# Kernel optimization log

Measured on AMD Instinct MI355X. Metric: run time of the kernel, lower is better.

Reference implementation:

```python
import jax, jax.numpy as jnp
import numpy as np

H = 1024; NH = 16; HD = H // NH  # hidden, heads, head_dim

def setup_inputs() -> dict:
    key = jax.random.key(0)
    ks = jax.random.split(key, 9)
    s = 1.0 / np.sqrt(H)
    return {
        "hidden_states": jax.random.normal(ks[0], (2, 2048, H), jnp.float32),
        "Wq": jax.random.uniform(ks[1], (H, H), jnp.float32, -s, s),
        "bq": jnp.zeros((H,), jnp.float32),
        "Wk": jax.random.uniform(ks[2], (H, H), jnp.float32, -s, s),
        "bk": jnp.zeros((H,), jnp.float32),
        "Wv": jax.random.uniform(ks[3], (H, H), jnp.float32, -s, s),
        "bv": jnp.zeros((H,), jnp.float32),
        "Wo": jax.random.uniform(ks[4], (H, H), jnp.float32, -s, s),
        "bo": jnp.zeros((H,), jnp.float32),
    }

def reference(hidden_states, Wq, bq, Wk, bk, Wv, bv, Wo, bo):
    B, S, _ = hidden_states.shape
    def heads(x):  # [B,S,H] -> [B,NH,S,HD]
        return x.reshape(B, S, NH, HD).transpose(0, 2, 1, 3)
    q = heads(hidden_states @ Wq + bq)
    k = heads(hidden_states @ Wk + bk)
    v = heads(hidden_states @ Wv + bv)
    scores = jnp.einsum('bhqd,bhkd->bhqk', q, k) / jnp.sqrt(jnp.float32(HD))
    causal = jnp.where(jnp.tril(jnp.ones((S, S), bool)), 0.0, -jnp.inf)
    probs = jax.nn.softmax(scores + causal[None, None], axis=-1)
    ctx = jnp.einsum('bhqk,bhkd->bhqd', probs, v)
    ctx = ctx.transpose(0, 2, 1, 3).reshape(B, S, H)
    return ctx @ Wo + bo
```

## Files before the change

### kernel.cpp

```cpp
#include <hip/hip_runtime.h>
#include <hip/hip_bf16.h>

#define BB 2
#define SS 2048
#define HH 1024
#define NHH 16
#define HDD 64
#define MM (BB*SS)
#define QKV_N (3*HH)

typedef _Float16 f16x8 __attribute__((ext_vector_type(8)));
typedef _Float16 f16x4 __attribute__((ext_vector_type(4)));
typedef float f32x4 __attribute__((ext_vector_type(4)));

#define MFMA16(a,b,c)  __builtin_amdgcn_mfma_f32_16x16x32_f16((a),(b),(c),0,0,0)
#define MFMA16K16(a,b,c) __builtin_amdgcn_mfma_f32_16x16x16f16((a),(b),(c),0,0,0)

__device__ __forceinline__ void gl2lds16(const _Float16* g, _Float16* l) {
    __builtin_amdgcn_global_load_lds(
        (const __attribute__((address_space(1))) void*)g,
        (__attribute__((address_space(3))) void*)l, 16, 0, 0);
}

__device__ __forceinline__ float fexp2(float x) { return __builtin_amdgcn_exp2f(x); }

__global__ __launch_bounds__(256) void prep_kernel(
    const float* __restrict__ X,
    const float* __restrict__ W0, const float* __restrict__ W1,
    const float* __restrict__ W2, const float* __restrict__ W3,
    _Float16* __restrict__ Xh,
    _Float16* __restrict__ WqkvT, _Float16* __restrict__ WoT)
{
    __shared__ float t[64][65];
    int z = blockIdx.z;
    int tid = threadIdx.x;
    if (z == 4) {
        int base = (blockIdx.y * 16 + blockIdx.x) * 256 + tid;
        const float4* xin = (const float4*)X;
        f16x4* xout = (f16x4*)Xh;
#pragma unroll
        for (int i = 0; i < 16; ++i) {
            float4 v = xin[base + i * 65536];
            f16x4 hh = {(_Float16)v.x, (_Float16)v.y, (_Float16)v.z, (_Float16)v.w};
            xout[base + i * 65536] = hh;
        }
        return;
    }
    const float* src = (z == 0) ? W0 : (z == 1) ? W1 : (z == 2) ? W2 : W3;
    _Float16* dst = (z < 3) ? (WqkvT + (size_t)z * HH * HH) : WoT;
    int k0 = blockIdx.y * 64, n0 = blockIdx.x * 64;
#pragma unroll
    for (int p = 0; p < 4; ++p) {
        int row = p * 16 + (tid >> 4);
        int col4 = (tid & 15) * 4;
        float4 v = *(const float4*)&src[(size_t)(k0 + row) * HH + n0 + col4];
        t[row][col4 + 0] = v.x; t[row][col4 + 1] = v.y;
        t[row][col4 + 2] = v.z; t[row][col4 + 3] = v.w;
    }
    __syncthreads();
#pragma unroll
    for (int p = 0; p < 2; ++p) {
        int nc = p * 32 + (tid >> 3);
        int ch = tid & 7;
        f16x8 o;
#pragma unroll
        for (int j = 0; j < 8; ++j) o[j] = (_Float16)t[ch * 8 + j][nc];
        *(f16x8*)&dst[(size_t)(n0 + nc) * HH + k0 + ch * 8] = o;
    }
}

__global__ __launch_bounds__(512, 2) void gemm_qkv_kernel(
    const _Float16* __restrict__ A, const _Float16* __restrict__ Bt,
    const float* __restrict__ bias0, const float* __restrict__ bias1, const float* __restrict__ bias2,
    _Float16* __restrict__ Qh, _Float16* __restrict__ Kh, _Float16* __restrict__ Vt)
{
    __shared__ _Float16 smem[65536];

    int bid = blockIdx.y * 12 + blockIdx.x;
    int swzb = (bid & 7) * 24 + (bid >> 3);
    int bx = swzb % 12, by = swzb / 12;
    int row0 = by * 256, n0 = bx * 256;

    int tid = threadIdx.x;
    int w = tid >> 6, l = tid & 63, m16 = l & 15, quad = l >> 4;
    int wm = w >> 2, wn = w & 3;

    int srow = w * 16 + (l >> 2);
    int sch = (l & 3) ^ ((l >> 2) & 3) ^ ((l >> 4) & 3);
    const _Float16* aptr = A + (size_t)(row0 + srow) * HH + sch * 8;
    const _Float16* bptr = Bt + (size_t)(n0 + srow) * HH + sch * 8;

    int gsw = (m16 & 3) ^ ((m16 >> 2) & 3);
    int acol = (quad ^ gsw) * 8;

    f32x4 zero4 = {0.f, 0.f, 0.f, 0.f};
    f32x4 acc[8][4];
#pragma unroll
    for (int i = 0; i < 8; ++i)
#pragma unroll
        for (int j = 0; j < 4; ++j) acc[i][j] = zero4;

    auto stageA = [&](int s, int h, int ks) {
        gl2lds16(aptr + (size_t)h * 128 * HH + s * 64 + ks * 32,
                 smem + (s & 1) * 16384 + ks * 8192 + (h * 128 + w * 16) * 32);
    };
    auto stageB = [&](int s, int h, int ks) {
        gl2lds16(bptr + (size_t)h * 128 * HH + s * 64 + ks * 32,
                 smem + 32768 + (s & 1) * 16384 + ks * 8192 + (h * 128 + w * 16) * 32);
    };

    stageA(0, 0, 0); stageA(0, 0, 1); stageA(0, 1, 0); stageA(0, 1, 1);
    stageB(0, 0, 0); stageB(0, 0, 1); stageB(0, 1, 0); stageB(0, 1, 1);

    for (int s = 0; s < 16; ++s) {
        const _Float16* Ab = smem + (s & 1) * 16384;
        const _Float16* Bb = smem + 32768 + (s & 1) * 16384;
        bool pf = (s + 1 < 16);
        f16x8 af[4][2], bf[2][2];

        if (pf) { stageA(s + 1, 0, 0); stageA(s + 1, 0, 1);
                  asm volatile("s_waitcnt vmcnt(2)" ::: "memory"); }
        else    { asm volatile("s_waitcnt vmcnt(0)" ::: "memory"); }
        asm volatile("s_barrier" ::: "memory");
#pragma unroll
        for (int fi = 0; fi < 4; ++fi)
#pragma unroll
            for (int ks = 0; ks < 2; ++ks)
                af[fi][ks] = *(const f16x8*)&Ab[ks * 8192 + (wm * 128 + fi * 16 + m16) * 32 + acol];
#pragma unroll
        for (int fj = 0; fj < 2; ++fj)
#pragma unroll
            for (int ks = 0; ks < 2; ++ks)
                bf[fj][ks] = *(const f16x8*)&Bb[ks * 8192 + (wn * 64 + fj * 16 + m16) * 32 + acol];
        __builtin_amdgcn_s_setprio(1);
#pragma unroll
        for (int fi = 0; fi < 4; ++fi)
#pragma unroll
            for (int fj = 0; fj < 2; ++fj) {
                acc[fi][fj] = MFMA16(af[fi][0], bf[fj][0], acc[fi][fj]);
                acc[fi][fj] = MFMA16(af[fi][1], bf[fj][1], acc[fi][fj]);
            }
        __builtin_amdgcn_s_setprio(0);
        asm volatile("s_barrier" ::: "memory");

        if (pf) { stageA(s + 1, 1, 0); stageA(s + 1, 1, 1); }
#pragma unroll
        for (int fj = 0; fj < 2; ++fj)
#pragma unroll
            for (int ks = 0; ks < 2; ++ks)
                bf[fj][ks] = *(const f16x8*)&Bb[ks * 8192 + (wn * 64 + 32 + fj * 16 + m16) * 32 + acol];
        __builtin_amdgcn_s_setprio(1);
#pragma unroll
        for (int fi = 0; fi < 4; ++fi)
#pragma unroll
            for (int fj = 0; fj < 2; ++fj) {
                acc[fi][2 + fj] = MFMA16(af[fi][0], bf[fj][0], acc[fi][2 + fj]);
                acc[fi][2 + fj] = MFMA16(af[fi][1], bf[fj][1], acc[fi][2 + fj]);
            }
        __builtin_amdgcn_s_setprio(0);
        asm volatile("s_barrier" ::: "memory");

        if (pf) { stageB(s + 1, 0, 0); stageB(s + 1, 0, 1); }
#pragma unroll
        for (int fi = 0; fi < 4; ++fi)
#pragma unroll
            for (int ks = 0; ks < 2; ++ks)
                af[fi][ks] = *(const f16x8*)&Ab[ks * 8192 + (wm * 128 + 64 + fi * 16 + m16) * 32 + acol];
        __builtin_amdgcn_s_setprio(1);
#pragma unroll
        for (int fi = 0; fi < 4; ++fi)
#pragma unroll
            for (int fj = 0; fj < 2; ++fj) {
                acc[4 + fi][2 + fj] = MFMA16(af[fi][0], bf[fj][0], acc[4 + fi][2 + fj]);
                acc[4 + fi][2 + fj] = MFMA16(af[fi][1], bf[fj][1], acc[4 + fi][2 + fj]);
            }
        __builtin_amdgcn_s_setprio(0);
        asm volatile("s_barrier" ::: "memory");

        if (pf) { stageB(s + 1, 1, 0); stageB(s + 1, 1, 1); }
#pragma unroll
        for (int fj = 0; fj < 2; ++fj)
#pragma unroll
            for (int ks = 0; ks < 2; ++ks)
                bf[fj][ks] = *(const f16x8*)&Bb[ks * 8192 + (wn * 64 + fj * 16 + m16) * 32 + acol];
        __builtin_amdgcn_s_setprio(1);
#pragma unroll
        for (int fi = 0; fi < 4; ++fi)
#pragma unroll
            for (int fj = 0; fj < 2; ++fj) {
                acc[4 + fi][fj] = MFMA16(af[fi][0], bf[fj][0], acc[4 + fi][fj]);
                acc[4 + fi][fj] = MFMA16(af[fi][1], bf[fj][1], acc[4 + fi][fj]);
            }
        __builtin_amdgcn_s_setprio(0);
        asm volatile("s_barrier" ::: "memory");
    }

    int which = n0 >> 10;
    const float* bias = (which == 0) ? bias0 : (which == 1) ? bias1 : bias2;
    int b = row0 >> 11, s0 = row0 & 2047;

#pragma unroll
    for (int rh = 0; rh < 2; ++rh) {
        __syncthreads();
        if (wm == rh) {
#pragma unroll
            for (int j = 0; j < 4; ++j) {
                int n_local = wn * 64 + j * 16 + m16;
                float bi = bias[(n0 + n_local) & 1023];
#pragma unroll
                for (int i = 0; i < 8; ++i)
#pragma unroll
                    for (int r = 0; r < 4; ++r) {
                        int m_loc = i * 16 + quad * 4 + r;
                        float v = acc[i][j][r] + bi;
                        if (which == 0) v *= 0.18033688011112042f;
                        if (which == 2) smem[n_local * 136 + m_loc] = (_Float16)v;
                        else            smem[m_loc * 264 + n_local] = (_Float16)v;
                    }
            }
        }
        __syncthreads();
        int hs0 = s0 + rh * 128;
        if (which == 2) {
#pragma unroll
            for (int p = 0; p < 8; ++p) {
                int n_local = p * 32 + (tid >> 4);
                int schunk = tid & 15;
                f16x8 v = *(const f16x8*)&smem[n_local * 136 + schunk * 8];
                int nw = (n0 + n_local) & 1023;
                int hh = nw >> 6, d = nw & 63;
                *(f16x8*)&Vt[((size_t)(b * NHH + hh) * HDD + d) * SS + hs0 + schunk * 8] = v;
            }
        } else {
            _Float16* dst = (which == 0) ? Qh : Kh;
            int hh0 = (n0 & 1023) >> 6;
#pragma unroll
            for (int p = 0; p < 8; ++p) {
                int m_local = p * 16 + (tid >> 5);
                int seg = tid & 31;
                f16x8 v = *(const f16x8*)&smem[m_local * 264 + seg * 8];
                int hh = hh0 + (seg >> 3), d = (seg & 7) * 8;
                *(f16x8*)&dst[((size_t)(b * NHH + hh) * SS + hs0 + m_local) * HDD + d] = v;
            }
        }
    }
}

__global__ __launch_bounds__(256) void gemm_out_kernel(
    const _Float16* __restrict__ A, const _Float16* __restrict__ Bt,
    const float* __restrict__ bias0, float* __restrict__ Out)
{
    const int K = HH;
    const int NT = K / 32;
    __shared__ _Float16 smem[24576];

    int row0 = blockIdx.y * 128, n0 = blockIdx.x * 128;
    int tid = threadIdx.x;
    int w = tid >> 6, l = tid & 63, m16 = l & 15, quad = l >> 4;
    int wm = w >> 1, wn = w & 1;

    int srow = w * 32 + (l >> 2);
    int sch = (l & 3) ^ ((l >> 2) & 3) ^ ((l >> 4) & 3);
    const _Float16* aptr = A + (size_t)(row0 + srow) * K + sch * 8;
    const _Float16* bptr = Bt + (size_t)(n0 + srow) * K + sch * 8;

    int gsw = (m16 & 3) ^ ((m16 >> 2) & 3);
    int acol = (quad ^ gsw) * 8;

    f32x4 zero4 = {0.f, 0.f, 0.f, 0.f};
    f32x4 acc[4][4];
#pragma unroll
    for (int i = 0; i < 4; ++i)
#pragma unroll
        for (int j = 0; j < 4; ++j) acc[i][j] = zero4;

    auto stage = [&](int t, int s) {
        int k0 = t * 32;
        int ao = s * 4096 + (w * 32) * 32;
        int bo = 12288 + s * 4096 + (w * 32) * 32;
        gl2lds16(aptr + k0, smem + ao);
        gl2lds16(aptr + (size_t)16 * K + k0, smem + ao + 16 * 32);
        gl2lds16(bptr + k0, smem + bo);
        gl2lds16(bptr + (size_t)16 * K + k0, smem + bo + 16 * 32);
    };

    stage(0, 0);
    stage(1, 1);
    int cur = 0;
    for (int t = 0; t < NT; ++t) {
        if (t < NT - 1) asm volatile("s_waitcnt vmcnt(4)" ::: "memory");
        else            asm volatile("s_waitcnt vmcnt(0)" ::: "memory");
        asm volatile("s_barrier" ::: "memory");
        if (t + 2 < NT) {
            int nxt = cur + 2; if (nxt >= 3) nxt -= 3;
            stage(t + 2, nxt);
        }
        const _Float16* Asr = smem + cur * 4096;
        const _Float16* Bsr = smem + 12288 + cur * 4096;
        f16x8 af[4], bf[4];
#pragma unroll
        for (int i = 0; i < 4; ++i)
            af[i] = *(const f16x8*)&Asr[(wm * 64 + i * 16 + m16) * 32 + acol];
#pragma unroll
        for (int j = 0; j < 4; ++j)
            bf[j] = *(const f16x8*)&Bsr[(wn * 64 + j * 16 + m16) * 32 + acol];
#pragma unroll
        for (int i = 0; i < 4; ++i)
#pragma unroll
            for (int j = 0; j < 4; ++j)
                acc[i][j] = MFMA16(af[i], bf[j], acc[i][j]);
        cur = (cur == 2) ? 0 : cur + 1;
    }

#pragma unroll
    for (int j = 0; j < 4; ++j) {
        int n = n0 + wn * 64 + j * 16 + m16;
        float bi = bias0[n];
#pragma unroll
        for (int i = 0; i < 4; ++i)
#pragma unroll
            for (int r = 0; r < 4; ++r) {
                int mg = row0 + wm * 64 + i * 16 + quad * 4 + r;
                Out[(size_t)mg * HH + n] = acc[i][j][r] + bi;
            }
    }
}

__global__ __launch_bounds__(512, 4) void attn_kernel(
    const _Float16* __restrict__ Qh, const _Float16* __restrict__ Kh,
    const _Float16* __restrict__ Vt, _Float16* __restrict__ Ctx)
{
    __shared__ _Float16 KV[3 * 8192];

    int tid = threadIdx.x;
    int w = tid >> 6, l = tid & 63;
    int m16 = l & 15, quad = l >> 4;
    int b = blockIdx.z, h = blockIdx.y;
    int tA = blockIdx.x, tB = 31 - tA;
    int half = w >> 2, wq = w & 3;
    int myT = half ? tB : tA;

    const _Float16* Q = Qh + (size_t)(b * NHH + h) * SS * HDD;
    const _Float16* K = Kh + (size_t)(b * NHH + h) * SS * HDD;
    const _Float16* V = Vt + (size_t)(b * NHH + h) * HDD * SS;

    int q = myT * 64 + wq * 16 + m16;
    f16x8 aq0 = *(const f16x8*)(Q + (size_t)q * HDD + quad * 8);
    f16x8 aq1 = *(const f16x8*)(Q + (size_t)q * HDD + 32 + quad * 8);

    int srow = w * 8 + (l >> 3);
    int sch = (l & 7) ^ (l >> 3);
    const _Float16* kg = K + (size_t)srow * HDD + sch * 8;
    const _Float16* vg = V + (size_t)srow * SS + sch * 8;

    auto stage = [&](int t, int s) {
        int kt = t * 64;
        _Float16* kb = &KV[s * 8192];
        _Float16* vb = &KV[s * 8192 + 4096];
        gl2lds16(kg + (size_t)kt * HDD, kb + (w * 8) * 64);
        gl2lds16(vg + kt, vb + (w * 8) * 64);
    };

    int swz = m16 & 7;
    int cka = (quad ^ swz) * 8;
    int ckb = ((quad + 4) ^ swz) * 8;
    int vco[4];
#pragma unroll
    for (int s = 0; s < 4; ++s)
        vco[s] = (((s * 2 + (quad >> 1)) ^ swz) * 8) + (quad & 1) * 4;

    f32x4 zero4 = {0.f, 0.f, 0.f, 0.f};
    const f16x4 ones4 = {(_Float16)1.f, (_Float16)1.f, (_Float16)1.f, (_Float16)1.f};
    f32x4 o[4];
#pragma unroll
    for (int c = 0; c < 4; ++c) o[c] = zero4;
    f32x4 lacc = zero4;

    stage(0, 0);
    stage(1, 1);
    int cur = 0;
    for (int t = 0; t <= tB; ++t) {
        int kt = t * 64;
        if (t < tB) asm volatile("s_waitcnt vmcnt(2)" ::: "memory");
        else        asm volatile("s_waitcnt vmcnt(0)" ::: "memory");
        asm volatile("s_barrier" ::: "memory");
        if (t + 2 <= tB) {
            int nxt = cur + 2; if (nxt >= 3) nxt -= 3;
            stage(t + 2, nxt);
        }

        if (t <= myT) {
            const _Float16* kb = &KV[cur * 8192];
            const _Float16* vb = &KV[cur * 8192 + 4096];
            f16x8 bk[4][2];
#pragma unroll
            for (int s = 0; s < 4; ++s) {
                const _Float16* kr = kb + (s * 16 + m16) * 64;
                bk[s][0] = *(const f16x8*)(kr + cka);
                bk[s][1] = *(const f16x8*)(kr + ckb);
            }
            f16x4 av[4][4];
#pragma unroll
            for (int c = 0; c < 4; ++c) {
                const _Float16* vr = vb + (c * 16 + m16) * 64;
#pragma unroll
                for (int s = 0; s < 4; ++s)
                    av[c][s] = *(const f16x4*)(vr + vco[s]);
            }

            f32x4 st[4];
#pragma unroll
            for (int s = 0; s < 4; ++s) {
                st[s] = MFMA16(bk[s][0], aq0, zero4);
                st[s] = MFMA16(bk[s][1], aq1, st[s]);
            }
            f16x4 pt[4];
            if (t == myT) {
#pragma unroll
                for (int s = 0; s < 4; ++s)
#pragma unroll
                    for (int r = 0; r < 4; ++r) {
                        float p = fexp2(st[s][r]);
                        int key = kt + s * 16 + quad * 4 + r;
                        if (key > q) p = 0.f;
                        pt[s][r] = (_Float16)p;
                    }
            } else {
#pragma unroll
                for (int s = 0; s < 4; ++s)
#pragma unroll
                    for (int r = 0; r < 4; ++r)
                        pt[s][r] = (_Float16)fexp2(st[s][r]);
            }
#pragma unroll
            for (int s = 0; s < 4; ++s)
                lacc = MFMA16K16(ones4, pt[s], lacc);
#pragma unroll
            for (int c = 0; c < 4; ++c)
#pragma unroll
                for (int s = 0; s < 4; ++s)
                    o[c] = MFMA16K16(av[c][s], pt[s], o[c]);
        }

        cur = (cur == 2) ? 0 : cur + 1;
    }

    float inv = 1.0f / lacc[0];
    size_t rowoff = ((size_t)(b * SS) + q) * HH + h * HDD;
#pragma unroll
    for (int c = 0; c < 4; ++c) {
        f16x4 ov;
#pragma unroll
        for (int r = 0; r < 4; ++r) ov[r] = (_Float16)(o[c][r] * inv);
        *(f16x4*)&Ctx[rowoff + c * 16 + quad * 4] = ov;
    }
}

extern "C" void kernel_launch(void* const* d_in, const int* in_sizes, int n_in,
                              void* d_out, int out_size, void* d_ws, size_t ws_size,
                              hipStream_t stream) {
    const float* hs = (const float*)d_in[0];
    const float* Wq = (const float*)d_in[1];
    const float* bq = (const float*)d_in[2];
    const float* Wk = (const float*)d_in[3];
    const float* bk = (const float*)d_in[4];
    const float* Wv = (const float*)d_in[5];
    const float* bv = (const float*)d_in[6];
    const float* Wo = (const float*)d_in[7];
    const float* bo = (const float*)d_in[8];
    float* out = (float*)d_out;

    size_t off = 0;
    auto alloc = [&](size_t bytes) {
        void* p = (char*)d_ws + off;
        off += (bytes + 255) & ~(size_t)255;
        return p;
    };
    _Float16* Xh    = (_Float16*)alloc((size_t)MM * HH * 2);
    _Float16* WqkvT = (_Float16*)alloc((size_t)3 * HH * HH * 2);
    _Float16* WoT   = (_Float16*)alloc((size_t)HH * HH * 2);
    _Float16* Qh    = (_Float16*)alloc((size_t)BB * NHH * SS * HDD * 2);
    _Float16* Kh    = (_Float16*)alloc((size_t)BB * NHH * SS * HDD * 2);
    _Float16* Vt    = (_Float16*)alloc((size_t)BB * NHH * SS * HDD * 2);
    _Float16* Ctx   = (_Float16*)alloc((size_t)MM * HH * 2);

    prep_kernel<<<dim3(16, 16, 5), 256, 0, stream>>>(
        hs, Wq, Wk, Wv, Wo, Xh, WqkvT, WoT);
    gemm_qkv_kernel<<<dim3(QKV_N / 256, MM / 256), 512, 0, stream>>>(
        Xh, WqkvT, bq, bk, bv, Qh, Kh, Vt);
    attn_kernel<<<dim3(16, NHH, BB), 512, 0, stream>>>(Qh, Kh, Vt, Ctx);
    gemm_out_kernel<<<dim3(HH / 128, MM / 128), 256, 0, stream>>>(
        Ctx, WoT, bo, out);
}
```

Before: 185.2 us.

## Retile QKV GEMM to 256x192 tiles for a 256-block grid

Changes the QKV projection GEMM tile from 256x256 to 256x192, so the grid grows from 192 to 256 blocks, which maps to one full wave across the 256 CUs. The inner loop is restructured to have each wave compute 8x3 fragments in four phases of 2 rows each, with partial B staging done only by waves 0-3. Because a tile can now straddle Q/K/V boundaries, the epilogue chooses bias and destination per column group. The aim is to remove the tail-wave underutilization, at the cost of less arithmetic reuse per tile and a more complex epilogue.

```diff
diff --git a/kernel.cpp b/kernel.cpp
--- a/kernel.cpp
+++ b/kernel.cpp
@@ -74,12 +74,12 @@
     const float* __restrict__ bias0, const float* __restrict__ bias1, const float* __restrict__ bias2,
     _Float16* __restrict__ Qh, _Float16* __restrict__ Kh, _Float16* __restrict__ Vt)
 {
-    __shared__ _Float16 smem[65536];
-
-    int bid = blockIdx.y * 12 + blockIdx.x;
-    int swzb = (bid & 7) * 24 + (bid >> 3);
-    int bx = swzb % 12, by = swzb / 12;
-    int row0 = by * 256, n0 = bx * 256;
+    __shared__ _Float16 smem[57344];
+
+    int bid = blockIdx.y * 16 + blockIdx.x;
+    int swzb = (bid & 7) * 32 + (bid >> 3);
+    int bx = swzb & 15, by = swzb >> 4;
+    int row0 = by * 256, n0 = bx * 192;
 
     int tid = threadIdx.x;
     int w = tid >> 6, l = tid & 63, m16 = l & 15, quad = l >> 4;
@@ -94,11 +94,11 @@
     int acol = (quad ^ gsw) * 8;
 
     f32x4 zero4 = {0.f, 0.f, 0.f, 0.f};
-    f32x4 acc[8][4];
+    f32x4 acc[8][3];
 #pragma unroll
     for (int i = 0; i < 8; ++i)
 #pragma unroll
-        for (int j = 0; j < 4; ++j) acc[i][j] = zero4;
+        for (int j = 0; j < 3; ++j) acc[i][j] = zero4;
 
     auto stageA = [&](int s, int h, int ks) {
         gl2lds16(aptr + (size_t)h * 128 * HH + s * 64 + ks * 32,
@@ -106,97 +106,69 @@
     };
     auto stageB = [&](int s, int h, int ks) {
         gl2lds16(bptr + (size_t)h * 128 * HH + s * 64 + ks * 32,
-                 smem + 32768 + (s & 1) * 16384 + ks * 8192 + (h * 128 + w * 16) * 32);
+                 smem + 32768 + (s & 1) * 12288 + ks * 6144 + (h * 128 + w * 16) * 32);
     };
 
     stageA(0, 0, 0); stageA(0, 0, 1); stageA(0, 1, 0); stageA(0, 1, 1);
-    stageB(0, 0, 0); stageB(0, 0, 1); stageB(0, 1, 0); stageB(0, 1, 1);
+    stageB(0, 0, 0); stageB(0, 0, 1);
+    if (w < 4) { stageB(0, 1, 0); stageB(0, 1, 1); }
 
     for (int s = 0; s < 16; ++s) {
         const _Float16* Ab = smem + (s & 1) * 16384;
-        const _Float16* Bb = smem + 32768 + (s & 1) * 16384;
+        const _Float16* Bb = smem + 32768 + (s & 1) * 12288;
         bool pf = (s + 1 < 16);
-        f16x8 af[4][2], bf[2][2];
+        f16x8 af[2][2], bf[3][2];
 
         if (pf) { stageA(s + 1, 0, 0); stageA(s + 1, 0, 1);
                   asm volatile("s_waitcnt vmcnt(2)" ::: "memory"); }
         else    { asm volatile("s_waitcnt vmcnt(0)" ::: "memory"); }
         asm volatile("s_barrier" ::: "memory");
 #pragma unroll
-        for (int fi = 0; fi < 4; ++fi)
+        for (int fj = 0; fj < 3; ++fj)
 #pragma unroll
             for (int ks = 0; ks < 2; ++ks)
-                af[fi][ks] = *(const f16x8*)&Ab[ks * 8192 + (wm * 128 + fi * 16 + m16) * 32 + acol];
-#pragma unroll
-        for (int fj = 0; fj < 2; ++fj)
+                bf[fj][ks] = *(const f16x8*)&Bb[ks * 6144 + (wn * 48 + fj * 16 + m16) * 32 + acol];
+#pragma unroll
+        for (int i = 0; i < 2; ++i)
 #pragma unroll
             for (int ks = 0; ks < 2; ++ks)
-                bf[fj][ks] = *(const f16x8*)&Bb[ks * 8192 + (wn * 64 + fj * 16 + m16) * 32 + acol];
+                af[i][ks] = *(const f16x8*)&Ab[ks * 8192 + (wm * 128 + i * 16 + m16) * 32 + acol];
         __builtin_amdgcn_s_setprio(1);
 #pragma unroll
-        for (int fi = 0; fi < 4; ++fi)
-#pragma unroll
-            for (int fj = 0; fj < 2; ++fj) {
-                acc[fi][fj] = MFMA16(af[fi][0], bf[fj][0], acc[fi][fj]);
-                acc[fi][fj] = MFMA16(af[fi][1], bf[fj][1], acc[fi][fj]);
+        for (int i = 0; i < 2; ++i)
+#pragma unroll
+            for (int fj = 0; fj < 3; ++fj) {
+                acc[i][fj] = MFMA16(af[i][0], bf[fj][0], acc[i][fj]);
+                acc[i][fj] = MFMA16(af[i][1], bf[fj][1], acc[i][fj]);
             }
         __builtin_amdgcn_s_setprio(0);
         asm volatile("s_barrier" ::: "memory");
 
-        if (pf) { stageA(s + 1, 1, 0); stageA(s + 1, 1, 1); }
-#pragma unroll
-        for (int fj = 0; fj < 2; ++fj)
-#pragma unroll
-            for (int ks = 0; ks < 2; ++ks)
-                bf[fj][ks] = *(const f16x8*)&Bb[ks * 8192 + (wn * 64 + 32 + fj * 16 + m16) * 32 + acol];
-        __builtin_amdgcn_s_setprio(1);
-#pragma unroll
-        for (int fi = 0; fi < 4; ++fi)
-#pragma unroll
-            for (int fj = 0; fj < 2; ++fj) {
-                acc[fi][2 + fj] = MFMA16(af[fi][0], bf[fj][0], acc[fi][2 + fj]);
-                acc[fi][2 + fj] = MFMA16(af[fi][1], bf[fj][1], acc[fi][2 + fj]);
-            }
-        __builtin_amdgcn_s_setprio(0);
-        asm volatile("s_barrier" ::: "memory");
-
-        if (pf) { stageB(s + 1, 0, 0); stageB(s + 1, 0, 1); }
-#pragma unroll
-        for (int fi = 0; fi < 4; ++fi)
-#pragma unroll
-            for (int ks = 0; ks < 2; ++ks)
-                af[fi][ks] = *(const f16x8*)&Ab[ks * 8192 + (wm * 128 + 64 + fi * 16 + m16) * 32 + acol];
-        __builtin_amdgcn_s_setprio(1);
-#pragma unroll
-        for (int fi = 0; fi < 4; ++fi)
-#pragma unroll
-            for (int fj = 0; fj < 2; ++fj) {
-                acc[4 + fi][2 + fj] = MFMA16(af[fi][0], bf[fj][0], acc[4 + fi][2 + fj]);
-                acc[4 + fi][2 + fj] = MFMA16(af[fi][1], bf[fj][1], acc[4 + fi][2 + fj]);
-            }
-        __builtin_amdgcn_s_setprio(0);
-        asm volatile("s_barrier" ::: "memory");
-
-        if (pf) { stageB(s + 1, 1, 0); stageB(s + 1, 1, 1); }
-#pragma unroll
-        for (int fj = 0; fj < 2; ++fj)
-#pragma unroll
-            for (int ks = 0; ks < 2; ++ks)
-                bf[fj][ks] = *(const f16x8*)&Bb[ks * 8192 + (wn * 64 + fj * 16 + m16) * 32 + acol];
-        __builtin_amdgcn_s_setprio(1);
-#pragma unroll
-        for (int fi = 0; fi < 4; ++fi)
-#pragma unroll
-            for (int fj = 0; fj < 2; ++fj) {
-                acc[4 + fi][fj] = MFMA16(af[fi][0], bf[fj][0], acc[4 + fi][fj]);
-                acc[4 + fi][fj] = MFMA16(af[fi][1], bf[fj][1], acc[4 + fi][fj]);
-            }
-        __builtin_amdgcn_s_setprio(0);
-        asm volatile("s_barrier" ::: "memory");
-    }
-
-    int which = n0 >> 10;
-    const float* bias = (which == 0) ? bias0 : (which == 1) ? bias1 : bias2;
+#pragma unroll
+        for (int p = 1; p < 4; ++p) {
+            if (pf) {
+                if (p == 1)      { stageA(s + 1, 1, 0); stageA(s + 1, 1, 1); }
+                else if (p == 2) { stageB(s + 1, 0, 0); stageB(s + 1, 0, 1); }
+                else if (w < 4)  { stageB(s + 1, 1, 0); stageB(s + 1, 1, 1); }
+            }
+#pragma unroll
+            for (int i = 0; i < 2; ++i)
+#pragma unroll
+                for (int ks = 0; ks < 2; ++ks)
+                    af[i][ks] = *(const f16x8*)&Ab[ks * 8192 + (wm * 128 + (2 * p + i) * 16 + m16) * 32 + acol];
+            __builtin_amdgcn_s_setprio(1);
+#pragma unroll
+            for (int i = 0; i < 2; ++i)
+#pragma unroll
+                for (int fj = 0; fj < 3; ++fj) {
+                    acc[2 * p + i][fj] = MFMA16(af[i][0], bf[fj][0], acc[2 * p + i][fj]);
+                    acc[2 * p + i][fj] = MFMA16(af[i][1], bf[fj][1], acc[2 * p + i][fj]);
+                }
+            __builtin_amdgcn_s_setprio(0);
+            asm volatile("s_barrier" ::: "memory");
+        }
+    }
+
     int b = row0 >> 11, s0 = row0 & 2047;
 
 #pragma unroll
@@ -204,42 +176,44 @@
         __syncthreads();
         if (wm == rh) {
 #pragma unroll
-            for (int j = 0; j < 4; ++j) {
-                int n_local = wn * 64 + j * 16 + m16;
-                float bi = bias[(n0 + n_local) & 1023];
+            for (int fj = 0; fj < 3; ++fj) {
+                int n_local = wn * 48 + fj * 16 + m16;
+                int n = n0 + n_local;
+                int which = n >> 10;
+                const float* bp = (which == 0) ? bias0 : (which == 1) ? bias1 : bias2;
+                float bi = bp[n & 1023];
 #pragma unroll
                 for (int i = 0; i < 8; ++i)
 #pragma unroll
                     for (int r = 0; r < 4; ++r) {
                         int m_loc = i * 16 + quad * 4 + r;
-                        float v = acc[i][j][r] + bi;
+                        float v = acc[i][fj][r] + bi;
                         if (which == 0) v *= 0.18033688011112042f;
-                        if (which == 2) smem[n_local * 136 + m_loc] = (_Float16)v;
-                        else            smem[m_loc * 264 + n_local] = (_Float16)v;
+                        if (which == 2) smem[25600 + n_local * 136 + m_loc] = (_Float16)v;
+                        else            smem[m_loc * 200 + n_local] = (_Float16)v;
                     }
             }
         }
         __syncthreads();
         int hs0 = s0 + rh * 128;
-        if (which == 2) {
-#pragma unroll
-            for (int p = 0; p < 8; ++p) {
-                int n_local = p * 32 + (tid >> 4);
-                int schunk = tid & 15;
-                f16x8 v = *(const f16x8*)&smem[n_local * 136 + schunk * 8];
-                int nw = (n0 + n_local) & 1023;
-                int hh = nw >> 6, d = nw & 63;
+#pragma unroll
+        for (int p = 0; p < 6; ++p) {
+            int idx = p * 512 + tid;
+            int m_local = idx / 24;
+            int cg = idx - m_local * 24;
+            int nc = n0 + cg * 8;
+            int which = nc >> 10;
+            if (which == 2) {
+                int nl = cg * 8 + (m_local & 7);
+                int schunk = m_local >> 3;
+                f16x8 v = *(const f16x8*)&smem[25600 + nl * 136 + schunk * 8];
+                int nn = n0 + nl;
+                int hh = (nn & 1023) >> 6, d = nn & 63;
                 *(f16x8*)&Vt[((size_t)(b * NHH + hh) * HDD + d) * SS + hs0 + schunk * 8] = v;
-            }
-        } else {
-            _Float16* dst = (which == 0) ? Qh : Kh;
-            int hh0 = (n0 & 1023) >> 6;
-#pragma unroll
-            for (int p = 0; p < 8; ++p) {
-                int m_local = p * 16 + (tid >> 5);
-                int seg = tid & 31;
-                f16x8 v = *(const f16x8*)&smem[m_local * 264 + seg * 8];
-                int hh = hh0 + (seg >> 3), d = (seg & 7) * 8;
+            } else {
+                f16x8 v = *(const f16x8*)&smem[m_local * 200 + cg * 8];
+                int hh = (nc & 1023) >> 6, d = nc & 63;
+                _Float16* dst = which ? Kh : Qh;
                 *(f16x8*)&dst[((size_t)(b * NHH + hh) * SS + hs0 + m_local) * HDD + d] = v;
             }
         }
@@ -486,7 +460,7 @@
 
     prep_kernel<<<dim3(16, 16, 5), 256, 0, stream>>>(
         hs, Wq, Wk, Wv, Wo, Xh, WqkvT, WoT);
-    gemm_qkv_kernel<<<dim3(QKV_N / 256, MM / 256), 512, 0, stream>>>(
+    gemm_qkv_kernel<<<dim3(16, 16), 512, 0, stream>>>(
         Xh, WqkvT, bq, bk, bv, Qh, Kh, Vt);
     attn_kernel<<<dim3(16, NHH, BB), 512, 0, stream>>>(Qh, Kh, Vt, Ctx);
     gemm_out_kernel<<<dim3(HH / 128, MM / 128), 256, 0, stream>>>(
```

New measurement: 180.9 us. 2.3% less time.
